# Optimization experiments

Measured on AMD Instinct MI355X. Metric: run time of the kernel, lower is better.

## Reference

```python
import jax, jax.numpy as jnp
import numpy as np

DIM = 2048
HEADS = 16
KV_HEADS = 4
DIM_HEAD = 128
INNER = HEADS * DIM_HEAD          # 2048
KV_INNER = KV_HEADS * DIM_HEAD    # 512
FF = 4 * DIM                      # 8192
QK_SCALE = 10.0                   # x-transformers default qk_norm_scale
B, S = 2, 2048


def layer_norm(x, g, b, eps=1e-5):
    m = jnp.mean(x, axis=-1, keepdims=True)
    v = jnp.mean((x - m) ** 2, axis=-1, keepdims=True)
    return (x - m) * jax.lax.rsqrt(v + eps) * g + b


def l2norm(t, eps=1e-12):
    n = jnp.sqrt(jnp.sum(t * t, axis=-1, keepdims=True))
    return t / jnp.maximum(n, eps)


def setup_inputs() -> dict:
    key = jax.random.key(0)
    ks = jax.random.split(key, 12)
    s = lambda fan_in: 1.0 / np.sqrt(fan_in)
    return {
        "x":     jax.random.normal(ks[0], (B, S, DIM), jnp.float32),
        "wq":    jax.random.normal(ks[1], (DIM, INNER), jnp.float32) * s(DIM),
        "wk":    jax.random.normal(ks[2], (DIM, KV_INNER), jnp.float32) * s(DIM),
        "wv":    jax.random.normal(ks[3], (DIM, KV_INNER), jnp.float32) * s(DIM),
        "wo":    jax.random.normal(ks[4], (INNER, DIM), jnp.float32) * s(INNER),
        "ln1_g": jnp.ones((DIM,), jnp.float32),
        "ln1_b": jnp.zeros((DIM,), jnp.float32),
        "w1":    jax.random.normal(ks[5], (DIM, FF), jnp.float32) * s(DIM),
        "b1":    jnp.zeros((FF,), jnp.float32),
        "lnf_g": jnp.ones((FF,), jnp.float32),
        "lnf_b": jnp.zeros((FF,), jnp.float32),
        "w2":    jax.random.normal(ks[6], (FF, DIM), jnp.float32) * s(FF),
        "b2":    jnp.zeros((DIM,), jnp.float32),
    }


def reference(x, wq, wk, wv, wo, ln1_g, ln1_b, w1, b1, lnf_g, lnf_b, w2, b2):
    b, s, _ = x.shape
    rep = HEADS // KV_HEADS
    # GQA projections
    q = (x @ wq).reshape(b, s, HEADS, DIM_HEAD).transpose(0, 2, 1, 3)      # [b,h,s,d]
    k = (x @ wk).reshape(b, s, KV_HEADS, DIM_HEAD).transpose(0, 2, 1, 3)   # [b,g,s,d]
    v = (x @ wv).reshape(b, s, KV_HEADS, DIM_HEAD).transpose(0, 2, 1, 3)
    # qk-norm: l2-normalize q/k along head dim, fixed scale
    q = l2norm(q)
    k = l2norm(k)
    k = jnp.repeat(k, rep, axis=1)  # expand kv heads to query heads
    v = jnp.repeat(v, rep, axis=1)
    scores = jnp.einsum("bhid,bhjd->bhij", q, k) * QK_SCALE
    attn = jax.nn.softmax(scores, axis=-1)
    o = jnp.einsum("bhij,bhjd->bhid", attn, v)
    o = o.transpose(0, 2, 1, 3).reshape(b, s, INNER) @ wo
    # post-attention LayerNorm (no residual in the source)
    h = layer_norm(o, ln1_g, ln1_b)
    # FFN: SiLU + post-activation LayerNorm (dropout inert in eval)
    f = jax.nn.silu(h @ w1 + b1)
    f = layer_norm(f, lnf_g, lnf_b)
    y = f @ w2 + b2
    # the source re-applies the SAME norm after the ffn
    return layer_norm(y, ln1_g, ln1_b)
```

## Files before the change

### kernel.cpp

```cpp
#include <hip/hip_runtime.h>


typedef __attribute__((ext_vector_type(8))) short short8;
typedef __attribute__((ext_vector_type(4))) float f32x4;
typedef __attribute__((ext_vector_type(16))) float f32x16;

__device__ __forceinline__ unsigned short f2bf(float f) {
  unsigned int u = __builtin_bit_cast(unsigned int, f);
  u += 0x7FFFu + ((u >> 16) & 1u);
  return (unsigned short)(u >> 16);
}
__device__ __forceinline__ float bf2f(unsigned short h) {
  unsigned int u = ((unsigned int)h) << 16;
  return __builtin_bit_cast(float, u);
}

typedef const void __attribute__((address_space(1)))* gas1_t;
typedef void __attribute__((address_space(3)))* las3_t;
#define GLDS16(g, l) \
  __builtin_amdgcn_global_load_lds((gas1_t)(const void*)(g), (las3_t)(void*)(l), 16, 0, 0)

__global__ __launch_bounds__(256) void cast_f32_bf16(const float* __restrict__ src,
                                                     unsigned short* __restrict__ dst,
                                                     int n) {
  int i = (blockIdx.x * 256 + threadIdx.x) * 4;
  if (i >= n) return;
  float4 f = *(const float4*)(src + i);
  uint2 u;
  u.x = (unsigned)f2bf(f.x) | ((unsigned)f2bf(f.y) << 16);
  u.y = (unsigned)f2bf(f.z) | ((unsigned)f2bf(f.w) << 16);
  *(uint2*)(dst + i) = u;
}

__global__ void transcast(const float* __restrict__ src, unsigned short* __restrict__ dst,
                          int R, int C, int dst_ld, int row_off) {
  __shared__ float t[32][33];
  const int tx = threadIdx.x, ty = threadIdx.y;
  const int c0 = blockIdx.x * 32, r0 = blockIdx.y * 32;
#pragma unroll
  for (int j = 0; j < 4; ++j)
    t[ty + j * 8][tx] = src[(size_t)(r0 + ty + j * 8) * C + c0 + tx];
  __syncthreads();
#pragma unroll
  for (int j = 0; j < 4; ++j)
    dst[(size_t)(row_off + c0 + ty + j * 8) * dst_ld + r0 + tx] = f2bf(t[tx][ty + j * 8]);
}

template <int KS>
__global__ __launch_bounds__(512, 1) void gemm8ph(const unsigned short* __restrict__ A,
                                                  const unsigned short* __restrict__ Bt,
                                                  unsigned short* __restrict__ C0,
                                                  unsigned short* __restrict__ C1,
                                                  int ldc, int Keff) {
  extern __shared__ char lds[];
  const int tid = threadIdx.x, l = tid & 63, w = tid >> 6;
  const int wr = w >> 2, wc = w & 3;
  const int gx = gridDim.x, gy = gridDim.y;
  const int did = blockIdx.y * gx + blockIdx.x;
  const int q = (gx * gy) >> 3;
  const int tcm = (did & 7) * q + (did >> 3);
  const int brow = (tcm % gy) * 256, bcol = (tcm / gy) * 256;
  const int ld = Keff * KS;
  const unsigned short* Aa = A + (size_t)brow * ld + blockIdx.z * Keff;
  const unsigned short* Bb = Bt + (size_t)bcol * ld + blockIdx.z * Keff;
  unsigned short* C = (KS == 1 || blockIdx.z == 0) ? C0 : C1;
  const int NT = Keff >> 6;

  const int slot = l >> 4;
  const int rowA = wr * 128 + (l & 15);
  const int aRd = ((((rowA << 2) | slot) << 4) ^ ((rowA & 7) << 4));
  const int rowB = wc * 64 + (l & 15);
  const int bRd = ((((rowB << 2) | slot) << 4) ^ ((rowB & 7) << 4));

  f32x4 acc[8][4];
#pragma unroll
  for (int m = 0; m < 8; ++m)
#pragma unroll
    for (int n = 0; n < 4; ++n) acc[m][n] = (f32x4){0.f, 0.f, 0.f, 0.f};

  auto stage = [&](int s) {
    const int tile = s >> 2, kind = s & 3;
    const int kofs = ((tile < NT) ? tile * 64 : 0) + (kind >> 1) * 32;
    const unsigned short* src = (kind & 1) ? Bb : Aa;
    char* dst = lds + (tile & 1) * 65536 + kind * 16384;
#pragma unroll
    for (int r = 0; r < 2; ++r) {
      const int g = r * 512 + tid;
      const int rw = ((g >> 3) << 1) | (((g >> 2) ^ (g >> 4)) & 1);
      const int sl = (g ^ rw) & 3;
      GLDS16(src + (size_t)rw * ld + kofs + sl * 8, dst + g * 16);
    }
  };

#define BAR() __builtin_amdgcn_s_barrier()
#define LGKM0() do { asm volatile("s_waitcnt lgkmcnt(0)" ::: "memory"); \
                     __builtin_amdgcn_sched_barrier(0); } while (0)
#define SBAR() __builtin_amdgcn_sched_barrier(0)
#define VM6() asm volatile("s_waitcnt vmcnt(6)" ::: "memory")
#define MFMA16(AF, BF, MO)                                                     \
  do {                                                                         \
    __builtin_amdgcn_s_setprio(1);                                             \
    _Pragma("unroll") for (int m_ = 0; m_ < 4; ++m_)                           \
        _Pragma("unroll") for (int n_ = 0; n_ < 4; ++n_)                       \
            acc[(MO) + m_][n_] = __builtin_amdgcn_mfma_f32_16x16x32_bf16(      \
                (AF)[m_], (BF)[n_], acc[(MO) + m_][n_], 0, 0, 0);              \
    __builtin_amdgcn_s_setprio(0);                                             \
  } while (0)

  short8 af0[4], af1[4], af2[4], af3[4], bf0[4], bf1[4];

  stage(0); stage(1); stage(2); stage(3); stage(4); stage(5);
  asm volatile("s_waitcnt vmcnt(8)" ::: "memory");
  BAR();
#pragma unroll
  for (int n = 0; n < 4; ++n) bf0[n] = *(const short8*)(lds + 16384 + bRd + n * 1024);
#pragma unroll
  for (int m = 0; m < 4; ++m) af0[m] = *(const short8*)(lds + aRd + m * 1024);

  for (int T = 0; T < NT; ++T) {
    char* cur = lds + (T & 1) * 65536;
    char* nxt = lds + ((T + 1) & 1) * 65536;
    char* A0 = cur, *A1 = cur + 32768, *B1 = cur + 49152;

    stage(4 * T + 6);
    BAR();
    LGKM0();
#pragma unroll
    for (int m = 0; m < 4; ++m) af1[m] = *(const short8*)(A0 + aRd + (4 + m) * 1024);
    SBAR();
    MFMA16(af0, bf0, 0);
    BAR();

    VM6();
    stage(4 * T + 7);
    BAR();
    LGKM0();
#pragma unroll
    for (int n = 0; n < 4; ++n) bf1[n] = *(const short8*)(B1 + bRd + n * 1024);
#pragma unroll
    for (int m = 0; m < 4; ++m) af2[m] = *(const short8*)(A1 + aRd + m * 1024);
    SBAR();
    MFMA16(af1, bf0, 4);
    BAR();

    stage(4 * T + 8);
    BAR();
    LGKM0();
#pragma unroll
    for (int m = 0; m < 4; ++m) af3[m] = *(const short8*)(A1 + aRd + (4 + m) * 1024);
    SBAR();
    MFMA16(af2, bf1, 0);
    BAR();

    VM6();
    stage(4 * T + 9);
    BAR();
    LGKM0();
#pragma unroll
    for (int n = 0; n < 4; ++n) bf0[n] = *(const short8*)(nxt + 16384 + bRd + n * 1024);
#pragma unroll
    for (int m = 0; m < 4; ++m) af0[m] = *(const short8*)(nxt + aRd + m * 1024);
    SBAR();
    MFMA16(af3, bf1, 4);
    BAR();
  }
#undef BAR
#undef LGKM0
#undef SBAR
#undef VM6
#undef MFMA16

#pragma unroll
  for (int m = 0; m < 8; ++m)
#pragma unroll
    for (int r = 0; r < 4; ++r) {
      const int row = brow + wr * 128 + m * 16 + (l >> 4) * 4 + r;
#pragma unroll
      for (int n = 0; n < 4; ++n) {
        const int col = bcol + wc * 64 + n * 16 + (l & 15);
        C[(size_t)row * ldc + col] = f2bf(acc[m][n][r]);
      }
    }
}

__global__ __launch_bounds__(256) void l2norm_qk(unsigned short* __restrict__ qkv) {
  const int wid = blockIdx.x * 4 + (threadIdx.x >> 6);
  const int l = threadIdx.x & 63;
  const int token = wid / 20, u = wid % 20;
  const int col = (u < 16) ? u * 128 : 2048 + (u - 16) * 128;
  unsigned short* p = qkv + (size_t)token * 3072 + col + l * 2;
  const float a = bf2f(p[0]), b = bf2f(p[1]);
  float ss = a * a + b * b;
#pragma unroll
  for (int m = 1; m < 64; m <<= 1) ss += __shfl_xor(ss, m);
  const float sc = ((u < 16) ? 10.f : 1.f) / fmaxf(sqrtf(ss), 1e-12f);
  p[0] = f2bf(a * sc);
  p[1] = f2bf(b * sc);
}

__global__ __launch_bounds__(256) void vtrans(const unsigned short* __restrict__ qkv,
                                              unsigned short* __restrict__ vt) {
  const int idx = blockIdx.x * 256 + threadIdx.x;
  const int s_ = idx & 2047;
  const int rest = idx >> 11;
  const int d = rest & 127;
  const int bg = rest >> 7;
  const int b = bg >> 2, g = bg & 3;
  vt[idx] = qkv[(size_t)(b * 2048 + s_) * 3072 + 2560 + g * 128 + d];
}

__global__ __launch_bounds__(512) void attn_kernel(const unsigned short* __restrict__ qkv,
                                                   const unsigned short* __restrict__ vt,
                                                   unsigned short* __restrict__ out) {
  extern __shared__ char smem[];
  const int tid = threadIdx.x, w = tid >> 6, l = tid & 63;
  const int hi = l >> 5, l31 = l & 31;

  const int n = blockIdx.x;
  const int np = (n & 7) * 32 + (n >> 3);
  const int qi = np & 7, bh = np >> 3;
  const int b = bh >> 4, h = bh & 15, g = h >> 2;
  const int q0 = qi * 256;

  const unsigned short* kbase = qkv + (size_t)(b * 2048) * 3072 + 2048 + g * 128;
  const unsigned short* vbase = vt + (size_t)(b * 4 + g) * 128 * 2048;

  short8 qf[8];
  {
    const unsigned short* qrow = qkv + (size_t)(b * 2048 + q0 + w * 32 + l31) * 3072 + h * 128;
#pragma unroll
    for (int st = 0; st < 8; ++st)
      qf[st] = *(const short8*)&qrow[st * 16 + hi * 8];
  }

  f32x16 o[4];
#pragma unroll
  for (int d0 = 0; d0 < 4; ++d0)
#pragma unroll
    for (int i = 0; i < 16; ++i) o[d0][i] = 0.f;
  float l_part = 0.f;

  const int krow = tid >> 3, kc = (tid & 7) * 2;
  const int vd = tid >> 2, vc = (tid & 3) * 2;
  const unsigned short* kg = kbase + (size_t)krow * 3072 + kc * 8;
  const unsigned short* vg = vbase + (size_t)vd * 2048 + vc * 8;
  const int ko0 = krow * 256 + ((kc ^ (krow & 15)) << 4);
  const int ko1 = krow * 256 + (((kc + 1) ^ (krow & 15)) << 4);
  const int vrp = vd >> 1, vcl = (vd & 1) * 8;
  const int vo0 = vrp * 256 + (((vcl + vc) ^ (vrp & 15)) << 4);
  const int vo1 = vrp * 256 + (((vcl + vc + 1) ^ (vrp & 15)) << 4);

  {
    uint4 k0 = *(const uint4*)kg, k1 = *(const uint4*)(kg + 8);
    uint4 v0 = *(const uint4*)vg, v1 = *(const uint4*)(vg + 8);
    char* Kb = smem;
    char* Vb = smem + 16384;
    *(uint4*)(Kb + ko0) = k0; *(uint4*)(Kb + ko1) = k1;
    *(uint4*)(Vb + vo0) = v0; *(uint4*)(Vb + vo1) = v1;
  }
  __syncthreads();

  const int swzk = l31 & 15;
  for (int t = 0; t < 32; ++t) {
    uint4 k0, k1, v0, v1;
    const bool more = (t + 1) < 32;
    if (more) {
      const size_t kvo = (size_t)(t + 1) * 64;
      k0 = *(const uint4*)(kg + kvo * 3072);
      k1 = *(const uint4*)(kg + kvo * 3072 + 8);
      v0 = *(const uint4*)(vg + kvo);
      v1 = *(const uint4*)(vg + kvo + 8);
    }

    char* Kb = smem + (t & 1) * 32768;
    char* Vb = Kb + 16384;

    f32x16 s0, s1;
#pragma unroll
    for (int i = 0; i < 16; ++i) { s0[i] = 0.f; s1[i] = 0.f; }
    __builtin_amdgcn_s_setprio(1);
#pragma unroll
    for (int st = 0; st < 8; ++st) {
      const int ch = st * 2 + hi;
      short8 kf0 = *(const short8*)(Kb + l31 * 256 + ((ch ^ swzk) << 4));
      short8 kf1 = *(const short8*)(Kb + (l31 + 32) * 256 + ((ch ^ swzk) << 4));
      s0 = __builtin_amdgcn_mfma_f32_32x32x16_bf16(kf0, qf[st], s0, 0, 0, 0);
      s1 = __builtin_amdgcn_mfma_f32_32x32x16_bf16(kf1, qf[st], s1, 0, 0, 0);
    }
    __builtin_amdgcn_s_setprio(0);

#pragma unroll
    for (int i = 0; i < 16; ++i) {
      s0[i] = __expf(s0[i] - 10.f);
      s1[i] = __expf(s1[i] - 10.f);
      l_part += s0[i] + s1[i];
    }

    short8 pa[4];
#pragma unroll
    for (int ks = 0; ks < 4; ++ks) {
      const f32x16& sv = (ks < 2) ? s0 : s1;
      const int base = (ks & 1) * 8;
      auto pk = [](float x, float y) -> unsigned {
        unsigned ux = __builtin_bit_cast(unsigned, x);
        unsigned uy = __builtin_bit_cast(unsigned, y);
        return ((uy + 0x8000u) & 0xFFFF0000u) | ((ux + 0x8000u) >> 16);
      };
      unsigned a = pk(sv[base + 0], sv[base + 1]);
      unsigned bq = pk(sv[base + 4], sv[base + 5]);
      unsigned c = pk(sv[base + 2], sv[base + 3]);
      unsigned d = pk(sv[base + 6], sv[base + 7]);
      unsigned as = __shfl_xor(a, 32), bs = __shfl_xor(bq, 32);
      unsigned cs = __shfl_xor(c, 32), ds = __shfl_xor(d, 32);
      uint4 wv;
      wv.x = (l < 32) ? a : bs;
      wv.y = (l < 32) ? c : ds;
      wv.z = (l < 32) ? as : bq;
      wv.w = (l < 32) ? cs : d;
      pa[ks] = __builtin_bit_cast(short8, wv);
    }

    __builtin_amdgcn_s_setprio(1);
#pragma unroll
    for (int ks = 0; ks < 4; ++ks) {
#pragma unroll
      for (int d0 = 0; d0 < 4; ++d0) {
        const int dd = d0 * 32 + l31;
        const int rp = dd >> 1;
        const int cl = ((dd & 1) * 8 + ks * 2 + hi) ^ (rp & 15);
        short8 vf = *(const short8*)(Vb + rp * 256 + (cl << 4));
        o[d0] = __builtin_amdgcn_mfma_f32_32x32x16_bf16(pa[ks], vf, o[d0], 0, 0, 0);
      }
    }
    __builtin_amdgcn_s_setprio(0);

    __syncthreads();
    if (more) {
      char* Kn = smem + ((t + 1) & 1) * 32768;
      char* Vn = Kn + 16384;
      *(uint4*)(Kn + ko0) = k0; *(uint4*)(Kn + ko1) = k1;
      *(uint4*)(Vn + vo0) = v0; *(uint4*)(Vn + vo1) = v1;
    }
    __syncthreads();
  }

  float ltot = l_part + __shfl_xor(l_part, 32);
  float linv = 1.f / ltot;
  const int tok_base = b * 2048 + q0 + w * 32;
#pragma unroll
  for (int r = 0; r < 16; ++r) {
    const int qr = (r & 3) + 8 * (r >> 2) + 4 * hi;
    const float li = __shfl(linv, qr);
    unsigned short* orow = out + (size_t)(tok_base + qr) * 2048 + h * 128 + l31;
#pragma unroll
    for (int d0 = 0; d0 < 4; ++d0)
      orow[d0 * 32] = f2bf(o[d0][r] * li);
  }
}

template <int NC, bool BIAS, bool SILU, bool OUTF32, bool SUM2>
__global__ __launch_bounds__(256) void ln_row(const unsigned short* __restrict__ src,
                                              const unsigned short* __restrict__ src2,
                                              unsigned short* __restrict__ dstb,
                                              float* __restrict__ dstf,
                                              const float* __restrict__ gamma,
                                              const float* __restrict__ beta,
                                              const float* __restrict__ bias) {
  constexpr int E = NC / 256;
  const int row = blockIdx.x, tid = threadIdx.x;
  const size_t base = (size_t)row * NC + tid * E;
  float v[E];
#pragma unroll
  for (int c = 0; c < E / 8; ++c) {
    uint4 u = *(const uint4*)(src + base + c * 8);
    const unsigned short* us = (const unsigned short*)&u;
#pragma unroll
    for (int j = 0; j < 8; ++j) v[c * 8 + j] = bf2f(us[j]);
  }
  if constexpr (SUM2) {
#pragma unroll
    for (int c = 0; c < E / 8; ++c) {
      uint4 u = *(const uint4*)(src2 + base + c * 8);
      const unsigned short* us = (const unsigned short*)&u;
#pragma unroll
      for (int j = 0; j < 8; ++j) v[c * 8 + j] += bf2f(us[j]);
    }
  }
  if constexpr (BIAS) {
#pragma unroll
    for (int i = 0; i < E; ++i) v[i] += bias[tid * E + i];
  }
  if constexpr (SILU) {
#pragma unroll
    for (int i = 0; i < E; ++i) v[i] = v[i] / (1.f + __expf(-v[i]));
  }
  float s = 0.f, q = 0.f;
#pragma unroll
  for (int i = 0; i < E; ++i) {
    s += v[i];
    q += v[i] * v[i];
  }
#pragma unroll
  for (int m = 1; m < 64; m <<= 1) {
    s += __shfl_xor(s, m);
    q += __shfl_xor(q, m);
  }
  __shared__ float rs[4], rq[4];
  if ((tid & 63) == 0) {
    rs[tid >> 6] = s;
    rq[tid >> 6] = q;
  }
  __syncthreads();
  s = rs[0] + rs[1] + rs[2] + rs[3];
  q = rq[0] + rq[1] + rq[2] + rq[3];
  const float mean = s / NC;
  const float rstd = rsqrtf(q / NC - mean * mean + 1e-5f);
#pragma unroll
  for (int i = 0; i < E; ++i)
    v[i] = (v[i] - mean) * rstd * gamma[tid * E + i] + beta[tid * E + i];
  if constexpr (OUTF32) {
#pragma unroll
    for (int c = 0; c < E / 4; ++c) {
      float4 f = {v[c * 4], v[c * 4 + 1], v[c * 4 + 2], v[c * 4 + 3]};
      *(float4*)(dstf + base + c * 4) = f;
    }
  } else {
#pragma unroll
    for (int c = 0; c < E / 8; ++c) {
      uint4 u;
      unsigned* up = (unsigned*)&u;
#pragma unroll
      for (int j = 0; j < 4; ++j)
        up[j] = (unsigned)f2bf(v[c * 8 + j * 2]) | ((unsigned)f2bf(v[c * 8 + j * 2 + 1]) << 16);
      *(uint4*)(dstb + base + c * 8) = u;
    }
  }
}

extern "C" void kernel_launch(void* const* d_in, const int* in_sizes, int n_in,
                              void* d_out, int out_size, void* d_ws, size_t ws_size,
                              hipStream_t stream) {
  (void)in_sizes; (void)n_in; (void)out_size; (void)ws_size;
  const float* x     = (const float*)d_in[0];
  const float* wq    = (const float*)d_in[1];
  const float* wk    = (const float*)d_in[2];
  const float* wv    = (const float*)d_in[3];
  const float* wo    = (const float*)d_in[4];
  const float* ln1_g = (const float*)d_in[5];
  const float* ln1_b = (const float*)d_in[6];
  const float* w1    = (const float*)d_in[7];
  const float* b1    = (const float*)d_in[8];
  const float* lnf_g = (const float*)d_in[9];
  const float* lnf_b = (const float*)d_in[10];
  const float* w2    = (const float*)d_in[11];
  const float* b2    = (const float*)d_in[12];

  unsigned short* ws = (unsigned short*)d_ws;
  unsigned short* wqkvT  = ws;
  unsigned short* woT    = wqkvT  + (size_t)3072 * 2048;
  unsigned short* w1T    = woT    + (size_t)2048 * 2048;
  unsigned short* w2T    = w1T    + (size_t)8192 * 2048;
  unsigned short* xb     = w2T    + (size_t)2048 * 8192;
  unsigned short* qkv    = xb     + (size_t)4096 * 2048;
  unsigned short* vt     = qkv    + (size_t)4096 * 3072;
  unsigned short* attn_o = vt     + (size_t)4096 * 512;
  unsigned short* f1     = attn_o + (size_t)4096 * 2048;

  (void)hipFuncSetAttribute((const void*)gemm8ph<1>,
                            hipFuncAttributeMaxDynamicSharedMemorySize, 131072);
  (void)hipFuncSetAttribute((const void*)gemm8ph<2>,
                            hipFuncAttributeMaxDynamicSharedMemorySize, 131072);
  (void)hipFuncSetAttribute((const void*)attn_kernel,
                            hipFuncAttributeMaxDynamicSharedMemorySize, 65536);

  const dim3 tb(32, 8);
  cast_f32_bf16<<<8192, 256, 0, stream>>>(x, xb, 4096 * 2048);
  transcast<<<dim3(64, 64),  tb, 0, stream>>>(wq, wqkvT, 2048, 2048, 2048, 0);
  transcast<<<dim3(16, 64),  tb, 0, stream>>>(wk, wqkvT, 2048, 512, 2048, 2048);
  transcast<<<dim3(16, 64),  tb, 0, stream>>>(wv, wqkvT, 2048, 512, 2048, 2560);
  transcast<<<dim3(64, 64),  tb, 0, stream>>>(wo, woT, 2048, 2048, 2048, 0);
  transcast<<<dim3(256, 64), tb, 0, stream>>>(w1, w1T, 2048, 8192, 2048, 0);
  transcast<<<dim3(64, 256), tb, 0, stream>>>(w2, w2T, 8192, 2048, 8192, 0);

  gemm8ph<1><<<dim3(12, 16, 1), 512, 131072, stream>>>(xb, wqkvT, qkv, nullptr, 3072, 2048);
  l2norm_qk<<<20480, 256, 0, stream>>>(qkv);
  vtrans<<<8192, 256, 0, stream>>>(qkv, vt);
  attn_kernel<<<256, 512, 65536, stream>>>(qkv, vt, attn_o);
  gemm8ph<2><<<dim3(8, 16, 2), 512, 131072, stream>>>(attn_o, woT, qkv, f1, 2048, 1024);
  ln_row<2048, false, false, false, true><<<4096, 256, 0, stream>>>(
      qkv, f1, xb, nullptr, ln1_g, ln1_b, nullptr);
  gemm8ph<1><<<dim3(32, 16, 1), 512, 131072, stream>>>(xb, w1T, f1, nullptr, 8192, 2048);
  ln_row<8192, true, true, false, false><<<4096, 256, 0, stream>>>(
      f1, nullptr, f1, nullptr, lnf_g, lnf_b, b1);
  gemm8ph<2><<<dim3(8, 16, 2), 512, 131072, stream>>>(f1, w2T, xb, attn_o, 2048, 4096);
  ln_row<2048, true, false, true, true><<<4096, 256, 0, stream>>>(
      xb, attn_o, nullptr, (float*)d_out, ln1_g, ln1_b, b2);
}
```

Measured before the change: 651.7 us.

## Split attention blocks into 128-query tiles of 256 threads, drop a barrier

Reshapes the attention launch from 256 blocks of 512 threads (256 queries each) to 512 blocks of 256 threads (128 queries each). Each thread now stages four 16-byte K and V chunks per tile instead of two. The barrier before writing the next double-buffered K/V tile is removed, leaving one barrier per iteration; the end-of-iteration barrier still orders reads and writes. Smaller blocks may let two blocks share a CU and improve scheduling, but K/V tiles are fetched twice as often overall and each thread holds more staging registers.

```diff
diff --git a/kernel.cpp b/kernel.cpp
--- a/kernel.cpp
+++ b/kernel.cpp
@@ -209,7 +209,7 @@
   vt[idx] = qkv[(size_t)(b * 2048 + s_) * 3072 + 2560 + g * 128 + d];
 }
 
-__global__ __launch_bounds__(512) void attn_kernel(const unsigned short* __restrict__ qkv,
+__global__ __launch_bounds__(256) void attn_kernel(const unsigned short* __restrict__ qkv,
                                                    const unsigned short* __restrict__ vt,
                                                    unsigned short* __restrict__ out) {
   extern __shared__ char smem[];
@@ -217,10 +217,10 @@
   const int hi = l >> 5, l31 = l & 31;
 
   const int n = blockIdx.x;
-  const int np = (n & 7) * 32 + (n >> 3);
-  const int qi = np & 7, bh = np >> 3;
+  const int np = (n & 7) * 64 + (n >> 3);
+  const int qi = np & 15, bh = np >> 4;
   const int b = bh >> 4, h = bh & 15, g = h >> 2;
-  const int q0 = qi * 256;
+  const int q0 = qi * 128;
 
   const unsigned short* kbase = qkv + (size_t)(b * 2048) * 3072 + 2048 + g * 128;
   const unsigned short* vbase = vt + (size_t)(b * 4 + g) * 128 * 2048;
@@ -240,36 +240,41 @@
     for (int i = 0; i < 16; ++i) o[d0][i] = 0.f;
   float l_part = 0.f;
 
-  const int krow = tid >> 3, kc = (tid & 7) * 2;
-  const int vd = tid >> 2, vc = (tid & 3) * 2;
+  const int krow = tid >> 2, kc = (tid & 3) * 4;
+  const int vd = tid >> 1, vc = (tid & 1) * 4;
   const unsigned short* kg = kbase + (size_t)krow * 3072 + kc * 8;
   const unsigned short* vg = vbase + (size_t)vd * 2048 + vc * 8;
-  const int ko0 = krow * 256 + ((kc ^ (krow & 15)) << 4);
-  const int ko1 = krow * 256 + (((kc + 1) ^ (krow & 15)) << 4);
-  const int vrp = vd >> 1, vcl = (vd & 1) * 8;
-  const int vo0 = vrp * 256 + (((vcl + vc) ^ (vrp & 15)) << 4);
-  const int vo1 = vrp * 256 + (((vcl + vc + 1) ^ (vrp & 15)) << 4);
-
+  int koff[4], voff[4];
   {
-    uint4 k0 = *(const uint4*)kg, k1 = *(const uint4*)(kg + 8);
-    uint4 v0 = *(const uint4*)vg, v1 = *(const uint4*)(vg + 8);
+    const int vrp = vd >> 1, vcl = (vd & 1) * 8;
+#pragma unroll
+    for (int i = 0; i < 4; ++i) {
+      koff[i] = krow * 256 + (((kc + i) ^ (krow & 15)) << 4);
+      voff[i] = vrp * 256 + (((vcl + vc + i) ^ (vrp & 15)) << 4);
+    }
+  }
+
+  {
     char* Kb = smem;
     char* Vb = smem + 16384;
-    *(uint4*)(Kb + ko0) = k0; *(uint4*)(Kb + ko1) = k1;
-    *(uint4*)(Vb + vo0) = v0; *(uint4*)(Vb + vo1) = v1;
+#pragma unroll
+    for (int i = 0; i < 4; ++i) *(uint4*)(Kb + koff[i]) = *(const uint4*)(kg + i * 8);
+#pragma unroll
+    for (int i = 0; i < 4; ++i) *(uint4*)(Vb + voff[i]) = *(const uint4*)(vg + i * 8);
   }
   __syncthreads();
 
   const int swzk = l31 & 15;
   for (int t = 0; t < 32; ++t) {
-    uint4 k0, k1, v0, v1;
+    uint4 kr[4], vr[4];
     const bool more = (t + 1) < 32;
     if (more) {
       const size_t kvo = (size_t)(t + 1) * 64;
-      k0 = *(const uint4*)(kg + kvo * 3072);
-      k1 = *(const uint4*)(kg + kvo * 3072 + 8);
-      v0 = *(const uint4*)(vg + kvo);
-      v1 = *(const uint4*)(vg + kvo + 8);
+#pragma unroll
+      for (int i = 0; i < 4; ++i) {
+        kr[i] = *(const uint4*)(kg + kvo * 3072 + i * 8);
+        vr[i] = *(const uint4*)(vg + kvo + i * 8);
+      }
     }
 
     char* Kb = smem + (t & 1) * 32768;
@@ -334,14 +339,15 @@
     }
     __builtin_amdgcn_s_setprio(0);
 
-    __syncthreads();
     if (more) {
       char* Kn = smem + ((t + 1) & 1) * 32768;
       char* Vn = Kn + 16384;
-      *(uint4*)(Kn + ko0) = k0; *(uint4*)(Kn + ko1) = k1;
-      *(uint4*)(Vn + vo0) = v0; *(uint4*)(Vn + vo1) = v1;
-    }
-    __syncthreads();
+#pragma unroll
+      for (int i = 0; i < 4; ++i) *(uint4*)(Kn + koff[i]) = kr[i];
+#pragma unroll
+      for (int i = 0; i < 4; ++i) *(uint4*)(Vn + voff[i]) = vr[i];
+      __syncthreads();
+    }
   }
 
   float ltot = l_part + __shfl_xor(l_part, 32);
@@ -485,7 +491,7 @@
   gemm8ph<1><<<dim3(12, 16, 1), 512, 131072, stream>>>(xb, wqkvT, qkv, nullptr, 3072, 2048);
   l2norm_qk<<<20480, 256, 0, stream>>>(qkv);
   vtrans<<<8192, 256, 0, stream>>>(qkv, vt);
-  attn_kernel<<<256, 512, 65536, stream>>>(qkv, vt, attn_o);
+  attn_kernel<<<512, 256, 65536, stream>>>(qkv, vt, attn_o);
   gemm8ph<2><<<dim3(8, 16, 2), 512, 131072, stream>>>(attn_o, woT, qkv, f1, 2048, 1024);
   ln_row<2048, false, false, false, true><<<4096, 256, 0, stream>>>(
       qkv, f1, xb, nullptr, ln1_g, ln1_b, nullptr);
```

After: 730.2 us. 12.0% more time.

## Split-K the QKV projection and vectorize weight transpose-cast with 64x64 tiles

Applied to the files above, without the earlier changes.

The QKV projection GEMM now runs with two K-splits, which raises the block count from 192 to 384 on a 256-CU device; the two bf16 partials are summed inside the existing l2norm and V-transpose kernels. The weight transpose-cast kernel moves to 64x64 tiles with float4 loads and 16-byte packed bf16 stores, cutting memory transactions on the large per-call weight conversion. In exchange there is an extra partial buffer write and read, and the QKV results carry slightly different rounding because two bf16 partials are added.

```diff
diff --git a/kernel.cpp b/kernel.cpp
--- a/kernel.cpp
+++ b/kernel.cpp
@@ -32,18 +32,31 @@
   *(uint2*)(dst + i) = u;
 }
 
-__global__ void transcast(const float* __restrict__ src, unsigned short* __restrict__ dst,
-                          int R, int C, int dst_ld, int row_off) {
-  __shared__ float t[32][33];
-  const int tx = threadIdx.x, ty = threadIdx.y;
-  const int c0 = blockIdx.x * 32, r0 = blockIdx.y * 32;
-#pragma unroll
-  for (int j = 0; j < 4; ++j)
-    t[ty + j * 8][tx] = src[(size_t)(r0 + ty + j * 8) * C + c0 + tx];
+__global__ __launch_bounds__(256) void transcast64(const float* __restrict__ src,
+                                                   unsigned short* __restrict__ dst,
+                                                   int R, int C, int dst_ld, int row_off) {
+  __shared__ float t[64][65];
+  const int tid = threadIdx.x;
+  const int tx = tid & 15, ty = tid >> 4;
+  const int c0 = blockIdx.x * 64, r0 = blockIdx.y * 64;
+#pragma unroll
+  for (int j = 0; j < 4; ++j) {
+    float4 v = *(const float4*)(src + (size_t)(r0 + j * 16 + ty) * C + c0 + tx * 4);
+    t[j * 16 + ty][tx * 4 + 0] = v.x;
+    t[j * 16 + ty][tx * 4 + 1] = v.y;
+    t[j * 16 + ty][tx * 4 + 2] = v.z;
+    t[j * 16 + ty][tx * 4 + 3] = v.w;
+  }
   __syncthreads();
-#pragma unroll
-  for (int j = 0; j < 4; ++j)
-    dst[(size_t)(row_off + c0 + ty + j * 8) * dst_ld + r0 + tx] = f2bf(t[tx][ty + j * 8]);
+  const int cc = tid >> 2, seg = tid & 3;
+  unsigned up[8];
+#pragma unroll
+  for (int i = 0; i < 8; ++i)
+    up[i] = (unsigned)f2bf(t[seg * 16 + 2 * i][cc]) |
+            ((unsigned)f2bf(t[seg * 16 + 2 * i + 1][cc]) << 16);
+  unsigned short* d = dst + (size_t)(row_off + c0 + cc) * dst_ld + r0 + seg * 16;
+  *(uint4*)(d) = *(uint4*)&up[0];
+  *(uint4*)(d + 8) = *(uint4*)&up[4];
 }
 
 template <int KS>
@@ -183,13 +196,17 @@
     }
 }
 
-__global__ __launch_bounds__(256) void l2norm_qk(unsigned short* __restrict__ qkv) {
+__global__ __launch_bounds__(256) void l2norm_qk(unsigned short* __restrict__ qkv,
+                                                 const unsigned short* __restrict__ p2) {
   const int wid = blockIdx.x * 4 + (threadIdx.x >> 6);
   const int l = threadIdx.x & 63;
   const int token = wid / 20, u = wid % 20;
   const int col = (u < 16) ? u * 128 : 2048 + (u - 16) * 128;
-  unsigned short* p = qkv + (size_t)token * 3072 + col + l * 2;
-  const float a = bf2f(p[0]), b = bf2f(p[1]);
+  const size_t off = (size_t)token * 3072 + col + l * 2;
+  unsigned short* p = qkv + off;
+  const unsigned short* q2 = p2 + off;
+  const float a = bf2f(p[0]) + bf2f(q2[0]);
+  const float b = bf2f(p[1]) + bf2f(q2[1]);
   float ss = a * a + b * b;
 #pragma unroll
   for (int m = 1; m < 64; m <<= 1) ss += __shfl_xor(ss, m);
@@ -199,6 +216,7 @@
 }
 
 __global__ __launch_bounds__(256) void vtrans(const unsigned short* __restrict__ qkv,
+                                              const unsigned short* __restrict__ p2,
                                               unsigned short* __restrict__ vt) {
   const int idx = blockIdx.x * 256 + threadIdx.x;
   const int s_ = idx & 2047;
@@ -206,7 +224,8 @@
   const int d = rest & 127;
   const int bg = rest >> 7;
   const int b = bg >> 2, g = bg & 3;
-  vt[idx] = qkv[(size_t)(b * 2048 + s_) * 3072 + 2560 + g * 128 + d];
+  const size_t src = (size_t)(b * 2048 + s_) * 3072 + 2560 + g * 128 + d;
+  vt[idx] = f2bf(bf2f(qkv[src]) + bf2f(p2[src]));
 }
 
 __global__ __launch_bounds__(512) void attn_kernel(const unsigned short* __restrict__ qkv,
@@ -473,18 +492,17 @@
   (void)hipFuncSetAttribute((const void*)attn_kernel,
                             hipFuncAttributeMaxDynamicSharedMemorySize, 65536);
 
-  const dim3 tb(32, 8);
   cast_f32_bf16<<<8192, 256, 0, stream>>>(x, xb, 4096 * 2048);
-  transcast<<<dim3(64, 64),  tb, 0, stream>>>(wq, wqkvT, 2048, 2048, 2048, 0);
-  transcast<<<dim3(16, 64),  tb, 0, stream>>>(wk, wqkvT, 2048, 512, 2048, 2048);
-  transcast<<<dim3(16, 64),  tb, 0, stream>>>(wv, wqkvT, 2048, 512, 2048, 2560);
-  transcast<<<dim3(64, 64),  tb, 0, stream>>>(wo, woT, 2048, 2048, 2048, 0);
-  transcast<<<dim3(256, 64), tb, 0, stream>>>(w1, w1T, 2048, 8192, 2048, 0);
-  transcast<<<dim3(64, 256), tb, 0, stream>>>(w2, w2T, 8192, 2048, 8192, 0);
-
-  gemm8ph<1><<<dim3(12, 16, 1), 512, 131072, stream>>>(xb, wqkvT, qkv, nullptr, 3072, 2048);
-  l2norm_qk<<<20480, 256, 0, stream>>>(qkv);
-  vtrans<<<8192, 256, 0, stream>>>(qkv, vt);
+  transcast64<<<dim3(32, 32),  256, 0, stream>>>(wq, wqkvT, 2048, 2048, 2048, 0);
+  transcast64<<<dim3(8, 32),   256, 0, stream>>>(wk, wqkvT, 2048, 512, 2048, 2048);
+  transcast64<<<dim3(8, 32),   256, 0, stream>>>(wv, wqkvT, 2048, 512, 2048, 2560);
+  transcast64<<<dim3(32, 32),  256, 0, stream>>>(wo, woT, 2048, 2048, 2048, 0);
+  transcast64<<<dim3(128, 32), 256, 0, stream>>>(w1, w1T, 2048, 8192, 2048, 0);
+  transcast64<<<dim3(32, 128), 256, 0, stream>>>(w2, w2T, 8192, 2048, 8192, 0);
+
+  gemm8ph<2><<<dim3(12, 16, 2), 512, 131072, stream>>>(xb, wqkvT, qkv, f1, 3072, 1024);
+  l2norm_qk<<<20480, 256, 0, stream>>>(qkv, f1);
+  vtrans<<<8192, 256, 0, stream>>>(qkv, f1, vt);
   attn_kernel<<<256, 512, 65536, stream>>>(qkv, vt, attn_o);
   gemm8ph<2><<<dim3(8, 16, 2), 512, 131072, stream>>>(attn_o, woT, qkv, f1, 2048, 1024);
   ln_row<2048, false, false, false, true><<<4096, 256, 0, stream>>>(
```

After: 669.6 us. 1.03x slower.
